# Kernel tuning notes

Measured on AMD Instinct MI355X. Metric: run time of the kernel, lower is better.

The kernel has to match this reference:

```python
import jax, jax.numpy as jnp
import numpy as np

MU = 1e-3   # step size for Omega_k (default mu=0.001)
RO = 1e-3   # step size for lagrange multipliers (default ro=0.001)


def setup_inputs() -> dict:
    key = jax.random.key(0)
    k1, k2, k3 = jax.random.split(key, 3)
    W, B, S, G, T = 4, 32, 16, 1024, 128  # windows, bins, SH coeffs, masked grid pts, time frames
    # SH basis evaluated on masked grid, broadcast to (W, B, S, G)
    Yp = jax.random.normal(k1, (W, B, S, G), dtype=jnp.float32) / np.sqrt(G)
    # Uk, Lambda_k come from SVD of the binaural signal Bk [W,B,S,T]
    Bk = jax.random.normal(k2, (W, B, S, T), dtype=jnp.float32)
    Uk, Lk, _ = jnp.linalg.svd(Bk, full_matrices=False)          # Uk: [W,B,S,S], Lk: [W,B,S]
    Lambda_k = jnp.eye(S, dtype=jnp.float32) * Lk[..., None, :]  # diag_embed -> [W,B,S,S]
    Omega_k0 = jax.random.normal(k3, (W, B, G, S), dtype=jnp.float32)
    return {"reduced_Yp": Yp, "Uk": Uk, "Lambda_k": Lambda_k,
            "Omega_k0": Omega_k0, "num_iterations": 20}


def reference(reduced_Yp, Uk, Lambda_k, Omega_k0, num_iterations):
    # GD_lagrange_multi with constraint_tol == 0 (the default dual-ascent path).
    W, B, S, G = reduced_Yp.shape
    target = jnp.matmul(Uk, Lambda_k)                 # [W,B,S,S], loop-invariant
    YpT = jnp.swapaxes(reduced_Yp, -1, -2)            # [W,B,G,S]
    lam0 = jnp.zeros((W, B, S, S), reduced_Yp.dtype)  # lagrange multipliers (S^2 flattened in torch)

    def step(carry, _):
        Omega, lam = carry
        # d/dOmega of sum ||Omega_row||_2: row-normalized Omega (norm over last dim, as in torch grad)
        norm = jnp.sqrt(jnp.sum(Omega * Omega, axis=-1, keepdims=True))  # [W,B,G,1]
        grad_omega = Omega / norm + jnp.matmul(YpT, lam)                 # [W,B,G,S]
        # constraint residual: Yp @ Omega - Uk @ Lambda  (computed with OLD Omega, as in source)
        grad_lam = jnp.matmul(reduced_Yp, Omega) - target                # [W,B,S,S]
        Omega = Omega - MU * grad_omega
        lam = lam + RO * grad_lam
        return (Omega, lam), None

    (Omega, lam), _ = jax.lax.scan(step, (Omega_k0, lam0), None, length=int(num_iterations))
    return Omega
```

## Files before the change

### kernel.cpp

```cpp
#include <hip/hip_runtime.h>


typedef float    f32x4 __attribute__((ext_vector_type(4)));
typedef _Float16 f16x4 __attribute__((ext_vector_type(4)));
typedef __fp16   h16x2 __attribute__((ext_vector_type(2)));

#define MUv 1e-3f
#define ROv 1e-3f

__device__ __forceinline__ f16x4 pack4(float a, float b, float c, float d) {
  h16x2 lo = __builtin_amdgcn_cvt_pkrtz(a, b);
  h16x2 hi = __builtin_amdgcn_cvt_pkrtz(c, d);
  union { struct { h16x2 lo, hi; } p; f16x4 v; } u;
  u.p.lo = lo; u.p.hi = hi;
  return u.v;
}

__global__ __launch_bounds__(1024) void gd_lagrange_kernel(
    const float* __restrict__ Yp,
    const float* __restrict__ Uk,
    const float* __restrict__ Lm,
    const float* __restrict__ Om0,
    const int* __restrict__ nitp,
    float* __restrict__ out) {
  constexpr int NT = 4, NW = 16;

  const int bid  = blockIdx.x;
  const int wb   = bid >> 1;
  const int hf   = bid & 1;
  const int tid  = threadIdx.x;
  const int wv   = tid >> 6;
  const int lane = tid & 63;
  const int q    = (tid >> 4) & 3;
  const int m    = tid & 15;
  const int g0   = wv * 64;

  __shared__ float ldsRed[NW][256];

  const float* ypg = Yp + (size_t)wb * 16384;
  const float* omg = Om0 + (size_t)wb * 16384;

  f32x4 rb[NT];
  #pragma unroll
  for (int t = 0; t < NT; ++t)
    rb[t] = *(const f32x4*)&ypg[m * 1024 + g0 + 16 * t + 4 * q];
  f32x4 Om[NT];
  #pragma unroll
  for (int t = 0; t < NT; ++t)
    #pragma unroll
    for (int r = 0; r < 4; ++r)
      Om[t][r] = omg[(g0 + 16 * t + 4 * q + r) * 16 + m];
  f32x4 tgt;
  {
    const float* uk = Uk + wb * 256;
    float Ld = Lm[wb * 256 + m * 17];
    #pragma unroll
    for (int e = 0; e < 4; ++e)
      tgt[e] = uk[(4 * q + e) * 16 + m] * Ld;
  }

  f16x4 Ifrag, ones1;
  #pragma unroll
  for (int e = 0; e < 4; ++e) {
    Ifrag[e] = (4 * q + e == m) ? (_Float16)1.0f : (_Float16)0.0f;
    ones1[e] = (_Float16)1.0f;
  }

  f16x4 YpB[NT], YpA[NT];
  #pragma unroll
  for (int t = 0; t < NT; ++t)
    YpB[t] = pack4(rb[t][0], rb[t][1], rb[t][2], rb[t][3]);
  #pragma unroll
  for (int t = 0; t < NT; ++t) {
    f32x4 z = {0.f, 0.f, 0.f, 0.f};
    f32x4 d = __builtin_amdgcn_mfma_f32_16x16x16f16(YpB[t], Ifrag, z, 0, 0, 0);
    YpA[t] = pack4(d[0], d[1], d[2], d[3]);
  }

  f16x4 OmB[NT];
  f32x4 uf[NT];
  #pragma unroll
  for (int t = 0; t < NT; ++t)
    OmB[t] = pack4(Om[t][0], Om[t][1], Om[t][2], Om[t][3]);
  #pragma unroll
  for (int t = 0; t < NT; ++t) {
    f32x4 z = {0.f, 0.f, 0.f, 0.f};
    f16x4 sq = OmB[t] * OmB[t];
    f32x4 d1 = __builtin_amdgcn_mfma_f32_16x16x16f16(sq, Ifrag, z, 0, 0, 0);
    f16x4 t1 = pack4(d1[0], d1[1], d1[2], d1[3]);
    f32x4 n2 = __builtin_amdgcn_mfma_f32_16x16x16f16(t1, ones1, z, 0, 0, 0);
    #pragma unroll
    for (int r = 0; r < 4; ++r)
      uf[t][r] = -MUv * __builtin_amdgcn_rsqf(n2[r]);
  }

  constexpr float SIG = 4096.f, ISIG = 1.f / 4096.f;
  f32x4 p0a = {0.f, 0.f, 0.f, 0.f}, p0b = {0.f, 0.f, 0.f, 0.f};
  f32x4 pua = {0.f, 0.f, 0.f, 0.f}, pub = {0.f, 0.f, 0.f, 0.f};
  #pragma unroll
  for (int t = 0; t < NT; ++t) {
    f16x4 OmU = pack4(SIG * uf[t][0] * Om[t][0], SIG * uf[t][1] * Om[t][1],
                      SIG * uf[t][2] * Om[t][2], SIG * uf[t][3] * Om[t][3]);
    if (t & 1) {
      p0b = __builtin_amdgcn_mfma_f32_16x16x16f16(YpB[t], OmB[t], p0b, 0, 0, 0);
      pub = __builtin_amdgcn_mfma_f32_16x16x16f16(YpB[t], OmU,    pub, 0, 0, 0);
    } else {
      p0a = __builtin_amdgcn_mfma_f32_16x16x16f16(YpB[t], OmB[t], p0a, 0, 0, 0);
      pua = __builtin_amdgcn_mfma_f32_16x16x16f16(YpB[t], OmU,    pua, 0, 0, 0);
    }
  }

  const int niter = nitp[0];
  const float Nf  = (float)niter;
  const float S1f = 0.5f * Nf * (Nf - 1.f);
  const float S2f = Nf * (Nf - 1.f) * (Nf - 2.f) * (1.f / 6.f);
  f32x4 Wpart = (f32x4)(S1f) * (p0a + p0b) + (f32x4)(S2f * ISIG) * (pua + pub);
  *(f32x4*)&ldsRed[wv][lane * 4] = Wpart;

  f32x4 cOm[NT];
  #pragma unroll
  for (int t = 0; t < NT; ++t) {
    #pragma unroll
    for (int r = 0; r < 4; ++r) {
      float base = 1.f + uf[t][r];
      float cn = 1.f;
      int n = niter;
      while (n) { if (n & 1) cn *= base; base *= base; n >>= 1; }
      cOm[t][r] = cn * Om[t][r];
    }
  }

  __syncthreads();

  if ((wv >> 3) == hf) {
    f32x4 s0 = {0.f,0.f,0.f,0.f}, s1 = {0.f,0.f,0.f,0.f},
          s2 = {0.f,0.f,0.f,0.f}, s3 = {0.f,0.f,0.f,0.f};
    #pragma unroll
    for (int w2 = 0; w2 < 4; ++w2) {
      s0 += *(const f32x4*)&ldsRed[w2][lane * 4];
      s1 += *(const f32x4*)&ldsRed[w2 + 4][lane * 4];
      s2 += *(const f32x4*)&ldsRed[w2 + 8][lane * 4];
      s3 += *(const f32x4*)&ldsRed[w2 + 12][lane * 4];
    }
    f32x4 S16 = ((s0 + s1) + (s2 + s3)) - (f32x4)(S1f) * tgt;
    constexpr float KLAM = -(MUv) * (ROv);
    f16x4 lamEff = pack4(KLAM * S16[0], KLAM * S16[1],
                         KLAM * S16[2], KLAM * S16[3]);

    float* og = out + (size_t)wb * 16384;
    #pragma unroll
    for (int t = 0; t < NT; ++t) {
      f32x4 o = __builtin_amdgcn_mfma_f32_16x16x16f16(YpA[t], lamEff, cOm[t], 0, 0, 0);
      #pragma unroll
      for (int r = 0; r < 4; ++r)
        og[(g0 + 16 * t + 4 * q + r) * 16 + m] = o[r];
    }
  }
}

extern "C" void kernel_launch(void* const* d_in, const int* in_sizes, int n_in,
                              void* d_out, int out_size, void* d_ws, size_t ws_size,
                              hipStream_t stream) {
  const float* Yp  = (const float*)d_in[0];
  const float* Uk  = (const float*)d_in[1];
  const float* Lm  = (const float*)d_in[2];
  const float* Om0 = (const float*)d_in[3];
  const int*   nit = (const int*)d_in[4];
  float* out = (float*)d_out;

  gd_lagrange_kernel<<<dim3(256), dim3(1024), 0, stream>>>(Yp, Uk, Lm, Om0, nit, out);
}
```

Measured before the change: 14.66 us.

## Split grid points across block pair and exchange partial sums through global workspace

```diff
diff --git a/kernel.cpp b/kernel.cpp
--- a/kernel.cpp
+++ b/kernel.cpp
@@ -2,11 +2,14 @@
 
 
 typedef float    f32x4 __attribute__((ext_vector_type(4)));
+typedef float    f32x2 __attribute__((ext_vector_type(2)));
 typedef _Float16 f16x4 __attribute__((ext_vector_type(4)));
 typedef __fp16   h16x2 __attribute__((ext_vector_type(2)));
 
 #define MUv 1e-3f
 #define ROv 1e-3f
+#define MAGIC 0x13579BDF
+#define WOFF 256
 
 __device__ __forceinline__ f16x4 pack4(float a, float b, float c, float d) {
   h16x2 lo = __builtin_amdgcn_cvt_pkrtz(a, b);
@@ -16,29 +19,44 @@
   return u.v;
 }
 
+__device__ __forceinline__ f32x2 h4_to_f2(f16x4 h) {
+  union { f16x4 h; f32x2 f; } u; u.h = h; return u.f;
+}
+
+__device__ __forceinline__ f32x4 f2_to_f4(f32x2 w) {
+  union { f32x2 f; f16x4 h; } u; u.f = w;
+  f32x4 r;
+  #pragma unroll
+  for (int e = 0; e < 4; ++e) r[e] = (float)u.h[e];
+  return r;
+}
+
 __global__ __launch_bounds__(1024) void gd_lagrange_kernel(
     const float* __restrict__ Yp,
     const float* __restrict__ Uk,
     const float* __restrict__ Lm,
     const float* __restrict__ Om0,
     const int* __restrict__ nitp,
-    float* __restrict__ out) {
-  constexpr int NT = 4, NW = 16;
+    float* __restrict__ out,
+    float* __restrict__ wsf) {
+  constexpr int NT = 2, NW = 16;
 
   const int bid  = blockIdx.x;
   const int wb   = bid >> 1;
   const int hf   = bid & 1;
+  const int pr_  = bid ^ 1;
   const int tid  = threadIdx.x;
   const int wv   = tid >> 6;
   const int lane = tid & 63;
   const int q    = (tid >> 4) & 3;
   const int m    = tid & 15;
-  const int g0   = wv * 64;
+  const int g0   = hf * 512 + wv * 32;
 
   __shared__ float ldsRed[NW][256];
 
   const float* ypg = Yp + (size_t)wb * 16384;
   const float* omg = Om0 + (size_t)wb * 16384;
+  int* flags = (int*)wsf;
 
   f32x4 rb[NT];
   #pragma unroll
@@ -132,29 +150,42 @@
 
   __syncthreads();
 
-  if ((wv >> 3) == hf) {
-    f32x4 s0 = {0.f,0.f,0.f,0.f}, s1 = {0.f,0.f,0.f,0.f},
-          s2 = {0.f,0.f,0.f,0.f}, s3 = {0.f,0.f,0.f,0.f};
-    #pragma unroll
-    for (int w2 = 0; w2 < 4; ++w2) {
-      s0 += *(const f32x4*)&ldsRed[w2][lane * 4];
-      s1 += *(const f32x4*)&ldsRed[w2 + 4][lane * 4];
-      s2 += *(const f32x4*)&ldsRed[w2 + 8][lane * 4];
-      s3 += *(const f32x4*)&ldsRed[w2 + 12][lane * 4];
-    }
-    f32x4 S16 = ((s0 + s1) + (s2 + s3)) - (f32x4)(S1f) * tgt;
-    constexpr float KLAM = -(MUv) * (ROv);
-    f16x4 lamEff = pack4(KLAM * S16[0], KLAM * S16[1],
-                         KLAM * S16[2], KLAM * S16[3]);
-
-    float* og = out + (size_t)wb * 16384;
-    #pragma unroll
-    for (int t = 0; t < NT; ++t) {
-      f32x4 o = __builtin_amdgcn_mfma_f32_16x16x16f16(YpA[t], lamEff, cOm[t], 0, 0, 0);
-      #pragma unroll
-      for (int r = 0; r < 4; ++r)
-        og[(g0 + 16 * t + 4 * q + r) * 16 + m] = o[r];
-    }
+  f32x4 s0 = {0.f,0.f,0.f,0.f}, s1 = {0.f,0.f,0.f,0.f},
+        s2 = {0.f,0.f,0.f,0.f}, s3 = {0.f,0.f,0.f,0.f};
+  #pragma unroll
+  for (int w2 = 0; w2 < 4; ++w2) {
+    s0 += *(const f32x4*)&ldsRed[w2][lane * 4];
+    s1 += *(const f32x4*)&ldsRed[w2 + 4][lane * 4];
+    s2 += *(const f32x4*)&ldsRed[w2 + 8][lane * 4];
+    s3 += *(const f32x4*)&ldsRed[w2 + 12][lane * 4];
+  }
+  f32x4 sown = (s0 + s1) + (s2 + s3);
+
+  if (wv == 0) {
+    *(f32x2*)&wsf[WOFF + bid * 128 + lane * 2] =
+        h4_to_f2(pack4(sown[0], sown[1], sown[2], sown[3]));
+    __threadfence();
+    if (lane == 0)
+      __hip_atomic_store(&flags[bid], MAGIC, __ATOMIC_RELEASE,
+                         __HIP_MEMORY_SCOPE_AGENT);
+  }
+
+  while (__hip_atomic_load(&flags[pr_], __ATOMIC_ACQUIRE,
+                           __HIP_MEMORY_SCOPE_AGENT) != MAGIC) {}
+  f32x4 wpart2 = f2_to_f4(*(const f32x2*)&wsf[WOFF + pr_ * 128 + lane * 2]);
+
+  f32x4 S16 = (sown + wpart2) - (f32x4)(S1f) * tgt;
+  constexpr float KLAM = -(MUv) * (ROv);
+  f16x4 lamEff = pack4(KLAM * S16[0], KLAM * S16[1],
+                       KLAM * S16[2], KLAM * S16[3]);
+
+  float* og = out + (size_t)wb * 16384;
+  #pragma unroll
+  for (int t = 0; t < NT; ++t) {
+    f32x4 o = __builtin_amdgcn_mfma_f32_16x16x16f16(YpA[t], lamEff, cOm[t], 0, 0, 0);
+    #pragma unroll
+    for (int r = 0; r < 4; ++r)
+      og[(g0 + 16 * t + 4 * q + r) * 16 + m] = o[r];
   }
 }
 
@@ -166,7 +197,9 @@
   const float* Lm  = (const float*)d_in[2];
   const float* Om0 = (const float*)d_in[3];
   const int*   nit = (const int*)d_in[4];
-  float* out = (float*)d_out;
-
-  gd_lagrange_kernel<<<dim3(256), dim3(1024), 0, stream>>>(Yp, Uk, Lm, Om0, nit, out);
-}
+  float* outp = (float*)d_out;
+  float* wsp  = (float*)d_ws;
+
+  gd_lagrange_kernel<<<dim3(256), dim3(1024), 0, stream>>>(
+      Yp, Uk, Lm, Om0, nit, outp, wsp);
+}
```

Result: slower. 48.76 us (+232.6%).
